# Optimization experiments

Hardware: AMD Instinct MI355X
Metric: run time of the kernel (lower is better)

Reference implementation:

```python
import jax, jax.numpy as jnp
import numpy as np

B, T, C, H = 2, 4096, 768, 12
HD = C // H  # head dim = 64


def setup_inputs() -> dict:
    key = jax.random.key(0)
    k1, k2, k3 = jax.random.split(key, 3)
    x = jax.random.normal(k1, (B, T, C), dtype=jnp.float32)
    # torch Linear stores weight as [out_features, in_features]
    w_attn = jax.random.normal(k2, (3 * C, C), dtype=jnp.float32) * (1.0 / np.sqrt(C))
    w_proj = jax.random.normal(k3, (C, C), dtype=jnp.float32) * (1.0 / np.sqrt(C))
    return {"x": x, "w_attn": w_attn, "w_proj": w_proj}


def reference(x, w_attn, w_proj):
    Bs, Ts, Cs = x.shape
    qkv = jnp.einsum('btc,oc->bto', x, w_attn)  # [B,T,3C]
    q, k, v = jnp.split(qkv, 3, axis=-1)
    # [B,H,T,HD]
    q = q.reshape(Bs, Ts, H, HD).transpose(0, 2, 1, 3)
    k = k.reshape(Bs, Ts, H, HD).transpose(0, 2, 1, 3)
    v = v.reshape(Bs, Ts, H, HD).transpose(0, 2, 1, 3)
    scores = jnp.einsum('bhqd,bhkd->bhqk', q, k) / jnp.sqrt(jnp.float32(HD))
    causal = jnp.tril(jnp.ones((Ts, Ts), dtype=bool))
    scores = jnp.where(causal[None, None, :, :], scores, -jnp.inf)
    att = jax.nn.softmax(scores, axis=-1)
    out = jnp.einsum('bhqk,bhkd->bhqd', att, v)  # [B,H,T,HD]
    out = out.transpose(0, 2, 1, 3).reshape(Bs, Ts, Cs)
    out = jnp.einsum('btc,oc->bto', out, w_proj)
    return out
```

## Files before the change

kernel.cpp:

```cpp
#include <hip/hip_runtime.h>
#include <hip/hip_bf16.h>
#include <cstdint>
#include <cstddef>

constexpr int B_ = 2, T_ = 4096, C_ = 768, H_ = 12, HD_ = 64;
constexpr int M_ = B_ * T_;
constexpr int NQKV_ = 3 * C_;

typedef __bf16 bf16_t;
typedef __bf16 bf16x8 __attribute__((ext_vector_type(8)));
typedef __bf16 bf16x4 __attribute__((ext_vector_type(4)));
typedef __bf16 bf16x2 __attribute__((ext_vector_type(2)));
typedef float  f32x4  __attribute__((ext_vector_type(4)));
typedef float  f32x16 __attribute__((ext_vector_type(16)));
typedef unsigned int u32;
typedef unsigned int u32x4 __attribute__((ext_vector_type(4)));

typedef const __attribute__((address_space(1))) void* gas_t;
typedef __attribute__((address_space(3))) void* las_t;

#define QSCALE 0.1803368801111204f

static __device__ __forceinline__ u32 pkbf16(float a, float b) {
  bf16x2 t;
  t[0] = (bf16_t)a;
  t[1] = (bf16_t)b;
  return __builtin_bit_cast(u32, t);
}

__global__ void cvt_f32_bf16_v4(const float* __restrict__ s,
                                bf16_t* __restrict__ d, int n4) {
  int i = blockIdx.x * blockDim.x + threadIdx.x;
  const int st = gridDim.x * blockDim.x;
  for (; i < n4; i += st) {
    const float4 v = reinterpret_cast<const float4*>(s)[i];
    bf16x4 o;
    o[0] = (bf16_t)v.x; o[1] = (bf16_t)v.y;
    o[2] = (bf16_t)v.z; o[3] = (bf16_t)v.w;
    reinterpret_cast<bf16x4*>(d)[i] = o;
  }
}

#define GEMM_CORE(Xb, Wb)                                                     \
  __shared__ __align__(16) char lds[32768];                                   \
  const int tid = threadIdx.x, lane = tid & 63, wave = tid >> 6;              \
  const int r16 = lane & 15, g = lane >> 4;                                   \
  const int wr = wave >> 1, wc = wave & 1;                                    \
  const int m0 = blockIdx.y * 128;                                            \
  const int n0 = blockIdx.x * 128;                                            \
  int prow[2], goff[2];                                                       \
  _Pragma("unroll")                                                           \
  for (int i = 0; i < 2; ++i) {                                               \
    const int p = (wave * 2 + i) * 64 + lane;                                 \
    prow[i] = p >> 2;                                                         \
    goff[i] = ((p & 3) ^ (prow[i] & 3)) * 8;                                  \
  }                                                                           \
  auto stage = [&](int buf, int k0) {                                         \
    char* const base = lds + buf * 16384;                                     \
    _Pragma("unroll")                                                         \
    for (int i = 0; i < 2; ++i) {                                             \
      __builtin_amdgcn_global_load_lds(                                       \
          (gas_t)(Xb + (size_t)prow[i] * C_ + k0 + goff[i]),                  \
          (las_t)(base + (wave * 2 + i) * 1024), 16, 0, 0);                   \
      __builtin_amdgcn_global_load_lds(                                       \
          (gas_t)(Wb + (size_t)prow[i] * C_ + k0 + goff[i]),                  \
          (las_t)(base + 8192 + (wave * 2 + i) * 1024), 16, 0, 0);            \
    }                                                                         \
  };                                                                          \
  f32x4 acc[4][4] = {};                                                       \
  const int kswz = (g ^ (r16 & 3)) * 16;                                      \
  stage(0, 0);                                                                \
  __syncthreads();                                                            \
  constexpr int KT = C_ / 32;                                                 \
  for (int kt = 0; kt < KT; ++kt) {                                           \
    if (kt + 1 < KT) stage((kt + 1) & 1, (kt + 1) * 32);                      \
    const char* Ab = lds + (kt & 1) * 16384;                                  \
    const char* Bb = Ab + 8192;                                               \
    bf16x8 a[4], b[4];                                                        \
    _Pragma("unroll")                                                         \
    for (int i = 0; i < 4; ++i)                                               \
      a[i] = *reinterpret_cast<const bf16x8*>(                                \
          Ab + (wr * 64 + i * 16 + r16) * 64 + kswz);                         \
    _Pragma("unroll")                                                         \
    for (int j = 0; j < 4; ++j)                                               \
      b[j] = *reinterpret_cast<const bf16x8*>(                                \
          Bb + (wc * 64 + j * 16 + r16) * 64 + kswz);                         \
    _Pragma("unroll")                                                         \
    for (int i = 0; i < 4; ++i)                                               \
      _Pragma("unroll")                                                       \
      for (int j = 0; j < 4; ++j)                                             \
        acc[i][j] = __builtin_amdgcn_mfma_f32_16x16x32_bf16(                  \
            a[i], b[j], acc[i][j], 0, 0, 0);                                  \
    __syncthreads();                                                          \
  }

__global__ __launch_bounds__(256) void gemm_qkv(
    const bf16_t* __restrict__ X, const bf16_t* __restrict__ W,
    bf16_t* __restrict__ Q, bf16_t* __restrict__ K, bf16_t* __restrict__ Vt) {
  GEMM_CORE(X + (size_t)blockIdx.y * 128 * C_,
            W + (size_t)blockIdx.x * 128 * C_)

#pragma unroll
  for (int j = 0; j < 4; ++j) {
    const int col = n0 + wc * 64 + j * 16 + r16;
    const int which = col / C_;
    const int c = col - which * C_;
    const int h = c >> 6, d = c & 63;
#pragma unroll
    for (int i = 0; i < 4; ++i) {
#pragma unroll
      for (int r = 0; r < 4; ++r) {
        const int row = m0 + wr * 64 + i * 16 + g * 4 + r;
        const int bb = row >> 12, t = row & (T_ - 1);
        const float v = acc[i][j][r];
        if (which == 0)
          Q[(((size_t)(bb * H_ + h)) * T_ + t) * HD_ + d] = (bf16_t)(v * QSCALE);
        else if (which == 1)
          K[(((size_t)(bb * H_ + h)) * T_ + t) * HD_ + d] = (bf16_t)v;
        else
          Vt[(((size_t)(bb * H_ + h)) * HD_ + d) * (size_t)T_ + t] = (bf16_t)v;
      }
    }
  }
}

__global__ __launch_bounds__(256) void gemm_proj(
    const bf16_t* __restrict__ A, const bf16_t* __restrict__ W,
    float* __restrict__ Out) {
  GEMM_CORE(A + (size_t)blockIdx.y * 128 * C_,
            W + (size_t)blockIdx.x * 128 * C_)

#pragma unroll
  for (int j = 0; j < 4; ++j) {
    const int col = n0 + wc * 64 + j * 16 + r16;
#pragma unroll
    for (int i = 0; i < 4; ++i)
#pragma unroll
      for (int r = 0; r < 4; ++r) {
        const int row = m0 + wr * 64 + i * 16 + g * 4 + r;
        Out[(size_t)row * C_ + col] = acc[i][j][r];
      }
  }
}

__global__ __launch_bounds__(256) void attn_fwd(
    const bf16_t* __restrict__ Q, const bf16_t* __restrict__ K,
    const bf16_t* __restrict__ Vt, bf16_t* __restrict__ O) {
  __shared__ __align__(16) char lds[32768];
  const int tid = threadIdx.x;
  const int lane = tid & 63, wave = tid >> 6;
  const int c32 = lane & 31, h = lane >> 5;
  const int bh = blockIdx.x;
  const int qt = gridDim.y - 1 - blockIdx.y;
  const int q0w = qt * 128 + wave * 32;

  const bf16_t* Qb = Q + (size_t)bh * T_ * HD_;
  const bf16_t* Kb = K + (size_t)bh * T_ * HD_;
  const bf16_t* Vb = Vt + (size_t)bh * HD_ * T_;

  bf16x8 qf[4];
#pragma unroll
  for (int dg = 0; dg < 4; ++dg)
    qf[dg] = *reinterpret_cast<const bf16x8*>(
        Qb + (size_t)(q0w + c32) * HD_ + dg * 16 + h * 8);

  bf16x8 ones;
#pragma unroll
  for (int j = 0; j < 8; ++j) ones[j] = (bf16_t)1.0f;

  f32x16 o0 = {}, o1 = {};
  f32x16 lac = {};

  const int srow0 = tid >> 3;
  const int srow1 = (tid + 256) >> 3;
  const int sck0 = (tid & 7) ^ (srow0 & 7);
  const int sck1 = (tid & 7) ^ (srow1 & 7);

  auto STAGE = [&](int t, int buf) {
    char* const kb = lds + buf * 16384;
    char* const vb = kb + 8192;
    __builtin_amdgcn_global_load_lds(
        (gas_t)(Kb + (size_t)(t * 64 + srow0) * HD_ + sck0 * 8),
        (las_t)(kb + wave * 1024), 16, 0, 0);
    __builtin_amdgcn_global_load_lds(
        (gas_t)(Kb + (size_t)(t * 64 + srow1) * HD_ + sck1 * 8),
        (las_t)(kb + 4096 + wave * 1024), 16, 0, 0);
    __builtin_amdgcn_global_load_lds(
        (gas_t)(Vb + (size_t)srow0 * T_ + t * 64 + sck0 * 8),
        (las_t)(vb + wave * 1024), 16, 0, 0);
    __builtin_amdgcn_global_load_lds(
        (gas_t)(Vb + (size_t)srow1 * T_ + t * 64 + sck1 * 8),
        (las_t)(vb + 4096 + wave * 1024), 16, 0, 0);
  };

  const int nt = qt * 2 + 2;
  STAGE(0, 0);
  __syncthreads();

  for (int t = 0; t < nt; ++t) {
    if (t + 1 < nt) STAGE(t + 1, (t + 1) & 1);
    const char* kl = lds + (t & 1) * 16384;
    const char* vl = kl + 8192;
#pragma unroll
    for (int ks = 0; ks < 2; ++ks) {
      const int kb0 = t * 64 + ks * 32;
      if (kb0 < q0w + 32) {
        f32x16 s = {};
#pragma unroll
        for (int dg = 0; dg < 4; ++dg) {
          const bf16x8 kf = *reinterpret_cast<const bf16x8*>(
              kl + (ks * 32 + c32) * 128 + (((dg * 2 + h) ^ (c32 & 7)) << 4));
          s = __builtin_amdgcn_mfma_f32_32x32x16_bf16(kf, qf[dg], s, 0, 0, 0);
        }
        if (kb0 + 31 > q0w) {
          const int qabs = q0w + c32;
          const int kbh = kb0 + 4 * h;
#pragma unroll
          for (int r = 0; r < 16; ++r) {
            if (kbh + (r & 3) + 8 * (r >> 2) > qabs) s[r] = -130.f;
          }
        }
#pragma unroll
        for (int r = 0; r < 16; ++r) s[r] = exp2f(s[r]);
        u32 X0 = pkbf16(s[0], s[1]),  X1 = pkbf16(s[2], s[3]);
        u32 X2 = pkbf16(s[4], s[5]),  X3 = pkbf16(s[6], s[7]);
        u32 X4 = pkbf16(s[8], s[9]),  X5 = pkbf16(s[10], s[11]);
        u32 X6 = pkbf16(s[12], s[13]), X7 = pkbf16(s[14], s[15]);
        const auto a0 = __builtin_amdgcn_permlane32_swap(X0, X2, false, false);
        const auto a1 = __builtin_amdgcn_permlane32_swap(X1, X3, false, false);
        const auto a2 = __builtin_amdgcn_permlane32_swap(X4, X6, false, false);
        const auto a3 = __builtin_amdgcn_permlane32_swap(X5, X7, false, false);
        const u32x4 w1 = {(u32)a0[0], (u32)a1[0], (u32)a0[1], (u32)a1[1]};
        const u32x4 w2 = {(u32)a2[0], (u32)a3[0], (u32)a2[1], (u32)a3[1]};
        const bf16x8 pa1 = __builtin_bit_cast(bf16x8, w1);
        const bf16x8 pa2 = __builtin_bit_cast(bf16x8, w2);
        lac = __builtin_amdgcn_mfma_f32_32x32x16_bf16(pa1, ones, lac, 0, 0, 0);
        lac = __builtin_amdgcn_mfma_f32_32x32x16_bf16(pa2, ones, lac, 0, 0, 0);
#pragma unroll
        for (int dgb = 0; dgb < 2; ++dgb) {
          const int vrow = dgb * 32 + c32;
          const bf16x8 vf0 = *reinterpret_cast<const bf16x8*>(
              vl + vrow * 128 + (((ks * 4 + h) ^ (c32 & 7)) << 4));
          const bf16x8 vf1 = *reinterpret_cast<const bf16x8*>(
              vl + vrow * 128 + (((ks * 4 + 2 + h) ^ (c32 & 7)) << 4));
          if (dgb == 0) {
            o0 = __builtin_amdgcn_mfma_f32_32x32x16_bf16(pa1, vf0, o0, 0, 0, 0);
            o0 = __builtin_amdgcn_mfma_f32_32x32x16_bf16(pa2, vf1, o0, 0, 0, 0);
          } else {
            o1 = __builtin_amdgcn_mfma_f32_32x32x16_bf16(pa1, vf0, o1, 0, 0, 0);
            o1 = __builtin_amdgcn_mfma_f32_32x32x16_bf16(pa2, vf1, o1, 0, 0, 0);
          }
        }
      }
    }
    __syncthreads();
  }

  const int b = bh / H_, hh = bh - b * H_;
#pragma unroll
  for (int r = 0; r < 16; ++r) {
    const int qr = (r & 3) + 8 * (r >> 2) + 4 * h;
    const float lr = 1.0f / lac[r];
    const size_t rowoff = ((size_t)(b * T_ + q0w + qr)) * C_ + hh * HD_;
    O[rowoff + c32] = (bf16_t)(o0[r] * lr);
    O[rowoff + 32 + c32] = (bf16_t)(o1[r] * lr);
  }
}

extern "C" void kernel_launch(void* const* d_in, const int* in_sizes, int n_in,
                              void* d_out, int out_size, void* d_ws,
                              size_t ws_size, hipStream_t stream) {
  const float* x  = (const float*)d_in[0];
  const float* wa = (const float*)d_in[1];
  const float* wp = (const float*)d_in[2];
  float* out = (float*)d_out;

  char* ws = (char*)d_ws;
  size_t off = 0;
  auto alloc = [&](size_t bytes) -> char* {
    char* p = ws + off;
    off += (bytes + 255) & ~(size_t)255;
    return p;
  };
  bf16_t* xb  = (bf16_t*)alloc((size_t)M_ * C_ * 2);
  bf16_t* wab = (bf16_t*)alloc((size_t)NQKV_ * C_ * 2);
  bf16_t* wpb = (bf16_t*)alloc((size_t)C_ * C_ * 2);
  bf16_t* Qb  = (bf16_t*)alloc((size_t)B_ * H_ * T_ * HD_ * 2);
  bf16_t* Kb  = (bf16_t*)alloc((size_t)B_ * H_ * T_ * HD_ * 2);
  bf16_t* Vtb = (bf16_t*)alloc((size_t)B_ * H_ * HD_ * T_ * 2);
  bf16_t* Ob  = (bf16_t*)alloc((size_t)M_ * C_ * 2);
  if (off > ws_size) return;

  cvt_f32_bf16_v4<<<512, 256, 0, stream>>>(x, xb, M_ * C_ / 4);
  cvt_f32_bf16_v4<<<512, 256, 0, stream>>>(wa, wab, NQKV_ * C_ / 4);
  cvt_f32_bf16_v4<<<256, 256, 0, stream>>>(wp, wpb, C_ * C_ / 4);

  gemm_qkv<<<dim3(NQKV_ / 128, M_ / 128), 256, 0, stream>>>(xb, wab, Qb, Kb, Vtb);
  attn_fwd<<<dim3(B_ * H_, T_ / 128), 256, 0, stream>>>(Qb, Kb, Vtb, Ob);
  gemm_proj<<<dim3(C_ / 128, M_ / 128), 256, 0, stream>>>(Ob, wpb, out);
}
```

Before: 210.3 us.

## Pair early and late causal query tiles per attention block for balanced work

Each attention block now handles two 64-row query tiles, one from the start of the sequence and its mirror from the end, so every block does about the same causal work. Blocks use 128 threads with each wave covering 32 rows of both tiles; one wave stages K and the other stages Vt into LDS. Each K fragment loaded from LDS is reused for both query tiles, and s_setprio is placed around the MFMA sections. The aim is to remove the tail imbalance of causal blocks and improve K/V reuse, at the cost of more registers per thread and a smaller grid of 768 blocks.

```diff
diff --git a/kernel.cpp b/kernel.cpp
--- a/kernel.cpp
+++ b/kernel.cpp
@@ -143,7 +143,7 @@
   }
 }
 
-__global__ __launch_bounds__(256) void attn_fwd(
+__global__ __launch_bounds__(128, 2) void attn_fwd(
     const bf16_t* __restrict__ Q, const bf16_t* __restrict__ K,
     const bf16_t* __restrict__ Vt, bf16_t* __restrict__ O) {
   __shared__ __align__(16) char lds[32768];
@@ -151,49 +151,45 @@
   const int lane = tid & 63, wave = tid >> 6;
   const int c32 = lane & 31, h = lane >> 5;
   const int bh = blockIdx.x;
-  const int qt = gridDim.y - 1 - blockIdx.y;
-  const int q0w = qt * 128 + wave * 32;
+  const int j = blockIdx.y;
+  const int qA0 = 64 * j + 32 * wave;
+  const int qB0 = 64 * (63 - j) + 32 * wave;
 
   const bf16_t* Qb = Q + (size_t)bh * T_ * HD_;
   const bf16_t* Kb = K + (size_t)bh * T_ * HD_;
   const bf16_t* Vb = Vt + (size_t)bh * HD_ * T_;
 
-  bf16x8 qf[4];
-#pragma unroll
-  for (int dg = 0; dg < 4; ++dg)
-    qf[dg] = *reinterpret_cast<const bf16x8*>(
-        Qb + (size_t)(q0w + c32) * HD_ + dg * 16 + h * 8);
+  bf16x8 qfA[4], qfB[4];
+#pragma unroll
+  for (int dg = 0; dg < 4; ++dg) {
+    qfA[dg] = *reinterpret_cast<const bf16x8*>(
+        Qb + (size_t)(qA0 + c32) * HD_ + dg * 16 + h * 8);
+    qfB[dg] = *reinterpret_cast<const bf16x8*>(
+        Qb + (size_t)(qB0 + c32) * HD_ + dg * 16 + h * 8);
+  }
 
   bf16x8 ones;
 #pragma unroll
-  for (int j = 0; j < 8; ++j) ones[j] = (bf16_t)1.0f;
-
-  f32x16 o0 = {}, o1 = {};
-  f32x16 lac = {};
-
-  const int srow0 = tid >> 3;
-  const int srow1 = (tid + 256) >> 3;
-  const int sck0 = (tid & 7) ^ (srow0 & 7);
-  const int sck1 = (tid & 7) ^ (srow1 & 7);
+  for (int q = 0; q < 8; ++q) ones[q] = (bf16_t)1.0f;
+
+  f32x16 o0A = {}, o1A = {}, lacA = {};
+  f32x16 o0B = {}, o1B = {}, lacB = {};
 
   auto STAGE = [&](int t, int buf) {
-    char* const kb = lds + buf * 16384;
-    char* const vb = kb + 8192;
-    __builtin_amdgcn_global_load_lds(
-        (gas_t)(Kb + (size_t)(t * 64 + srow0) * HD_ + sck0 * 8),
-        (las_t)(kb + wave * 1024), 16, 0, 0);
-    __builtin_amdgcn_global_load_lds(
-        (gas_t)(Kb + (size_t)(t * 64 + srow1) * HD_ + sck1 * 8),
-        (las_t)(kb + 4096 + wave * 1024), 16, 0, 0);
-    __builtin_amdgcn_global_load_lds(
-        (gas_t)(Vb + (size_t)srow0 * T_ + t * 64 + sck0 * 8),
-        (las_t)(vb + wave * 1024), 16, 0, 0);
-    __builtin_amdgcn_global_load_lds(
-        (gas_t)(Vb + (size_t)srow1 * T_ + t * 64 + sck1 * 8),
-        (las_t)(vb + 4096 + wave * 1024), 16, 0, 0);
+    char* const base = lds + buf * 16384 + wave * 8192;
+#pragma unroll
+    for (int i = 0; i < 8; ++i) {
+      const int r = i * 8 + (lane >> 3);
+      const int c = (lane & 7) ^ (r & 7);
+      const bf16_t* p = (wave == 0)
+          ? Kb + (size_t)(t * 64 + r) * HD_ + c * 8
+          : Vb + (size_t)r * T_ + t * 64 + c * 8;
+      __builtin_amdgcn_global_load_lds((gas_t)p, (las_t)(base + i * 1024),
+                                       16, 0, 0);
+    }
   };
 
-  const int nt = qt * 2 + 2;
+  const int nt = 64 - j;
   STAGE(0, 0);
   __syncthreads();
 
@@ -204,38 +200,77 @@
 #pragma unroll
     for (int ks = 0; ks < 2; ++ks) {
       const int kb0 = t * 64 + ks * 32;
-      if (kb0 < q0w + 32) {
-        f32x16 s = {};
-#pragma unroll
-        for (int dg = 0; dg < 4; ++dg) {
-          const bf16x8 kf = *reinterpret_cast<const bf16x8*>(
+      if (kb0 < qB0 + 32) {
+        const bool actA = kb0 < qA0 + 32;
+        bf16x8 kf[4];
+#pragma unroll
+        for (int dg = 0; dg < 4; ++dg)
+          kf[dg] = *reinterpret_cast<const bf16x8*>(
               kl + (ks * 32 + c32) * 128 + (((dg * 2 + h) ^ (c32 & 7)) << 4));
-          s = __builtin_amdgcn_mfma_f32_32x32x16_bf16(kf, qf[dg], s, 0, 0, 0);
+        f32x16 sB = {};
+        __builtin_amdgcn_s_setprio(1);
+#pragma unroll
+        for (int dg = 0; dg < 4; ++dg)
+          sB = __builtin_amdgcn_mfma_f32_32x32x16_bf16(kf[dg], qfB[dg], sB,
+                                                       0, 0, 0);
+        __builtin_amdgcn_s_setprio(0);
+        if (kb0 + 31 > qB0) {
+          const int qabs = qB0 + c32;
+          const int kbh = kb0 + 4 * h;
+#pragma unroll
+          for (int r = 0; r < 16; ++r)
+            if (kbh + (r & 3) + 8 * (r >> 2) > qabs) sB[r] = -130.f;
         }
-        if (kb0 + 31 > q0w) {
-          const int qabs = q0w + c32;
-          const int kbh = kb0 + 4 * h;
-#pragma unroll
-          for (int r = 0; r < 16; ++r) {
-            if (kbh + (r & 3) + 8 * (r >> 2) > qabs) s[r] = -130.f;
+#pragma unroll
+        for (int r = 0; r < 16; ++r) sB[r] = exp2f(sB[r]);
+        u32 Y0 = pkbf16(sB[0], sB[1]),  Y1 = pkbf16(sB[2], sB[3]);
+        u32 Y2 = pkbf16(sB[4], sB[5]),  Y3 = pkbf16(sB[6], sB[7]);
+        u32 Y4 = pkbf16(sB[8], sB[9]),  Y5 = pkbf16(sB[10], sB[11]);
+        u32 Y6 = pkbf16(sB[12], sB[13]), Y7 = pkbf16(sB[14], sB[15]);
+        auto b0 = __builtin_amdgcn_permlane32_swap(Y0, Y2, false, false);
+        auto b1 = __builtin_amdgcn_permlane32_swap(Y1, Y3, false, false);
+        auto b2 = __builtin_amdgcn_permlane32_swap(Y4, Y6, false, false);
+        auto b3 = __builtin_amdgcn_permlane32_swap(Y5, Y7, false, false);
+        const u32x4 wB1 = {(u32)b0[0], (u32)b1[0], (u32)b0[1], (u32)b1[1]};
+        const u32x4 wB2 = {(u32)b2[0], (u32)b3[0], (u32)b2[1], (u32)b3[1]};
+        const bf16x8 paB1 = __builtin_bit_cast(bf16x8, wB1);
+        const bf16x8 paB2 = __builtin_bit_cast(bf16x8, wB2);
+        lacB = __builtin_amdgcn_mfma_f32_32x32x16_bf16(paB1, ones, lacB, 0, 0, 0);
+        lacB = __builtin_amdgcn_mfma_f32_32x32x16_bf16(paB2, ones, lacB, 0, 0, 0);
+        bf16x8 paA1, paA2;
+        if (actA) {
+          f32x16 sA = {};
+          __builtin_amdgcn_s_setprio(1);
+#pragma unroll
+          for (int dg = 0; dg < 4; ++dg)
+            sA = __builtin_amdgcn_mfma_f32_32x32x16_bf16(kf[dg], qfA[dg], sA,
+                                                         0, 0, 0);
+          __builtin_amdgcn_s_setprio(0);
+          if (kb0 + 31 > qA0) {
+            const int qabs = qA0 + c32;
+            const int kbh = kb0 + 4 * h;
+#pragma unroll
+            for (int r = 0; r < 16; ++r)
+              if (kbh + (r & 3) + 8 * (r >> 2) > qabs) sA[r] = -130.f;
           }
+#pragma unroll
+          for (int r = 0; r < 16; ++r) sA[r] = exp2f(sA[r]);
+          u32 Z0 = pkbf16(sA[0], sA[1]),  Z1 = pkbf16(sA[2], sA[3]);
+          u32 Z2 = pkbf16(sA[4], sA[5]),  Z3 = pkbf16(sA[6], sA[7]);
+          u32 Z4 = pkbf16(sA[8], sA[9]),  Z5 = pkbf16(sA[10], sA[11]);
+          u32 Z6 = pkbf16(sA[12], sA[13]), Z7 = pkbf16(sA[14], sA[15]);
+          auto a0 = __builtin_amdgcn_permlane32_swap(Z0, Z2, false, false);
+          auto a1 = __builtin_amdgcn_permlane32_swap(Z1, Z3, false, false);
+          auto a2 = __builtin_amdgcn_permlane32_swap(Z4, Z6, false, false);
+          auto a3 = __builtin_amdgcn_permlane32_swap(Z5, Z7, false, false);
+          const u32x4 wA1 = {(u32)a0[0], (u32)a1[0], (u32)a0[1], (u32)a1[1]};
+          const u32x4 wA2 = {(u32)a2[0], (u32)a3[0], (u32)a2[1], (u32)a3[1]};
+          paA1 = __builtin_bit_cast(bf16x8, wA1);
+          paA2 = __builtin_bit_cast(bf16x8, wA2);
+          lacA = __builtin_amdgcn_mfma_f32_32x32x16_bf16(paA1, ones, lacA, 0, 0, 0);
+          lacA = __builtin_amdgcn_mfma_f32_32x32x16_bf16(paA2, ones, lacA, 0, 0, 0);
         }
-#pragma unroll
-        for (int r = 0; r < 16; ++r) s[r] = exp2f(s[r]);
-        u32 X0 = pkbf16(s[0], s[1]),  X1 = pkbf16(s[2], s[3]);
-        u32 X2 = pkbf16(s[4], s[5]),  X3 = pkbf16(s[6], s[7]);
-        u32 X4 = pkbf16(s[8], s[9]),  X5 = pkbf16(s[10], s[11]);
-        u32 X6 = pkbf16(s[12], s[13]), X7 = pkbf16(s[14], s[15]);
-        const auto a0 = __builtin_amdgcn_permlane32_swap(X0, X2, false, false);
-        const auto a1 = __builtin_amdgcn_permlane32_swap(X1, X3, false, false);
-        const auto a2 = __builtin_amdgcn_permlane32_swap(X4, X6, false, false);
-        const auto a3 = __builtin_amdgcn_permlane32_swap(X5, X7, false, false);
-        const u32x4 w1 = {(u32)a0[0], (u32)a1[0], (u32)a0[1], (u32)a1[1]};
-        const u32x4 w2 = {(u32)a2[0], (u32)a3[0], (u32)a2[1], (u32)a3[1]};
-        const bf16x8 pa1 = __builtin_bit_cast(bf16x8, w1);
-        const bf16x8 pa2 = __builtin_bit_cast(bf16x8, w2);
-        lac = __builtin_amdgcn_mfma_f32_32x32x16_bf16(pa1, ones, lac, 0, 0, 0);
-        lac = __builtin_amdgcn_mfma_f32_32x32x16_bf16(pa2, ones, lac, 0, 0, 0);
+        __builtin_amdgcn_s_setprio(1);
 #pragma unroll
         for (int dgb = 0; dgb < 2; ++dgb) {
           const int vrow = dgb * 32 + c32;
@@ -244,13 +279,22 @@
           const bf16x8 vf1 = *reinterpret_cast<const bf16x8*>(
               vl + vrow * 128 + (((ks * 4 + 2 + h) ^ (c32 & 7)) << 4));
           if (dgb == 0) {
-            o0 = __builtin_amdgcn_mfma_f32_32x32x16_bf16(pa1, vf0, o0, 0, 0, 0);
-            o0 = __builtin_amdgcn_mfma_f32_32x32x16_bf16(pa2, vf1, o0, 0, 0, 0);
+            o0B = __builtin_amdgcn_mfma_f32_32x32x16_bf16(paB1, vf0, o0B, 0, 0, 0);
+            o0B = __builtin_amdgcn_mfma_f32_32x32x16_bf16(paB2, vf1, o0B, 0, 0, 0);
+            if (actA) {
+              o0A = __builtin_amdgcn_mfma_f32_32x32x16_bf16(paA1, vf0, o0A, 0, 0, 0);
+              o0A = __builtin_amdgcn_mfma_f32_32x32x16_bf16(paA2, vf1, o0A, 0, 0, 0);
+            }
           } else {
-            o1 = __builtin_amdgcn_mfma_f32_32x32x16_bf16(pa1, vf0, o1, 0, 0, 0);
-            o1 = __builtin_amdgcn_mfma_f32_32x32x16_bf16(pa2, vf1, o1, 0, 0, 0);
+            o1B = __builtin_amdgcn_mfma_f32_32x32x16_bf16(paB1, vf0, o1B, 0, 0, 0);
+            o1B = __builtin_amdgcn_mfma_f32_32x32x16_bf16(paB2, vf1, o1B, 0, 0, 0);
+            if (actA) {
+              o1A = __builtin_amdgcn_mfma_f32_32x32x16_bf16(paA1, vf0, o1A, 0, 0, 0);
+              o1A = __builtin_amdgcn_mfma_f32_32x32x16_bf16(paA2, vf1, o1A, 0, 0, 0);
+            }
           }
         }
+        __builtin_amdgcn_s_setprio(0);
       }
     }
     __syncthreads();
@@ -260,10 +304,14 @@
 #pragma unroll
   for (int r = 0; r < 16; ++r) {
     const int qr = (r & 3) + 8 * (r >> 2) + 4 * h;
-    const float lr = 1.0f / lac[r];
-    const size_t rowoff = ((size_t)(b * T_ + q0w + qr)) * C_ + hh * HD_;
-    O[rowoff + c32] = (bf16_t)(o0[r] * lr);
-    O[rowoff + 32 + c32] = (bf16_t)(o1[r] * lr);
+    const float lrA = 1.0f / lacA[r];
+    const float lrB = 1.0f / lacB[r];
+    const size_t rowA = ((size_t)(b * T_ + qA0 + qr)) * C_ + hh * HD_;
+    const size_t rowB = ((size_t)(b * T_ + qB0 + qr)) * C_ + hh * HD_;
+    O[rowA + c32] = (bf16_t)(o0A[r] * lrA);
+    O[rowA + 32 + c32] = (bf16_t)(o1A[r] * lrA);
+    O[rowB + c32] = (bf16_t)(o0B[r] * lrB);
+    O[rowB + 32 + c32] = (bf16_t)(o1B[r] * lrB);
   }
 }
 
@@ -296,6 +344,6 @@
   cvt_f32_bf16_v4<<<256, 256, 0, stream>>>(wp, wpb, C_ * C_ / 4);
 
   gemm_qkv<<<dim3(NQKV_ / 128, M_ / 128), 256, 0, stream>>>(xb, wab, Qb, Kb, Vtb);
-  attn_fwd<<<dim3(B_ * H_, T_ / 128), 256, 0, stream>>>(Qb, Kb, Vtb, Ob);
+  attn_fwd<<<dim3(B_ * H_, 32), 128, 0, stream>>>(Qb, Kb, Vtb, Ob);
   gemm_proj<<<dim3(C_ / 128, M_ / 128), 256, 0, stream>>>(Ob, wpb, out);
 }
```

New measurement: 227.0 us. 7.9% more time.
